# Performance work log

Hardware: AMD Instinct MI355X
Metric: run time of the kernel (lower is better)

The kernel has to match this reference:

```python
import jax, jax.numpy as jnp
import numpy as np

E, T, D_IN, D_H = 8, 4096, 2048, 1408

def setup_inputs() -> dict:
    key = jax.random.key(0)
    k_x, k_g, k_d, k_u = jax.random.split(key, 4)
    x = jax.random.normal(k_x, (E, T, D_IN), dtype=jnp.float32)
    gate_proj = jax.random.normal(k_g, (E, D_IN, D_H), dtype=jnp.float32) * 0.02
    down_proj = jax.random.normal(k_d, (E, D_IN, D_H), dtype=jnp.float32) * 0.02
    up_proj = jax.random.normal(k_u, (E, D_H, D_IN), dtype=jnp.float32) * 0.02
    return {"x": x, "gate_proj": gate_proj, "down_proj": down_proj,
            "up_proj": up_proj, "tokens_per_expert": T}

def reference(x, gate_proj, down_proj, up_proj, tokens_per_expert):
    # ep_size == 1 -> dispatch/combine are identity; x: [E, T, dim_in]
    # SwiGLU: h = silu(x @ gate) * (x @ down); out = h @ up
    h = jax.nn.silu(jnp.einsum('etd,edh->eth', x, gate_proj)) \
        * jnp.einsum('etd,edh->eth', x, down_proj)
    out = jnp.einsum('eth,ehd->etd', h, up_proj)
    return out
```

## Files before the change

kernel.cpp:

```cpp
#include <hip/hip_runtime.h>
#include <hip/hip_bf16.h>


typedef __bf16 bf16x8 __attribute__((ext_vector_type(8)));
typedef float  f32x4  __attribute__((ext_vector_type(4)));

__device__ __forceinline__ void gload16(const void* g, void* l) {
  __builtin_amdgcn_global_load_lds((const __attribute__((address_space(1))) void*)g,
                                   (__attribute__((address_space(3))) void*)l,
                                   16, 0, 0);
}

__device__ __forceinline__ unsigned short f2bf(float f) {
  union { float fv; unsigned u; } v; v.fv = f;
  unsigned r = (v.u + 0x7fffu + ((v.u >> 16) & 1u)) >> 16;
  return (unsigned short)r;
}

__global__ __launch_bounds__(256)
void cvt_f32_bf16(const float* __restrict__ in, unsigned short* __restrict__ out,
                  long n) {
  long i = ((long)blockIdx.x * 256 + threadIdx.x) * 4;
  const long stride = (long)gridDim.x * 1024;
  for (; i < n; i += stride) {
    const float4 v = *(const float4*)(in + i);
    ushort4 o;
    o.x = f2bf(v.x); o.y = f2bf(v.y); o.z = f2bf(v.z); o.w = f2bf(v.w);
    *(ushort4*)(out + i) = o;
  }
}

__global__ __launch_bounds__(256)
void trcvt(const float* __restrict__ in, unsigned short* __restrict__ out,
           int R, int C) {
  __shared__ unsigned short tile[32][33];
  const float* src = in + (size_t)blockIdx.z * R * C;
  unsigned short* dst = out + (size_t)blockIdx.z * R * C;
  const int c0 = blockIdx.x << 5, r0 = blockIdx.y << 5;
  const int tx = threadIdx.x, ty = threadIdx.y;
#pragma unroll
  for (int i = 0; i < 32; i += 8)
    tile[ty + i][tx] = f2bf(src[(size_t)(r0 + ty + i) * C + (c0 + tx)]);
  __syncthreads();
#pragma unroll
  for (int i = 0; i < 32; i += 8)
    dst[(size_t)(c0 + ty + i) * R + (r0 + tx)] = tile[tx][ty + i];
}

template <int KDIM, int NDIM, bool FUSED, bool F32OUT>
__global__ __launch_bounds__(512, 2)
void gemm_ring(const unsigned short* __restrict__ A,
               const unsigned short* __restrict__ B0,
               const unsigned short* __restrict__ B1,
               void* __restrict__ Cout) {
  constexpr int BN   = FUSED ? 128 : 256;
  constexpr int NB_N = NDIM / BN;
  constexpr int NS   = KDIM / 32;
  constexpr int SLOT = 16384;

  __shared__ __align__(16) unsigned short lds[4 * SLOT];

  const int t = threadIdx.x;
  const int w = t >> 6;
  const int lane = t & 63;
  const int e = blockIdx.y;

  const int cpx = gridDim.x >> 3;
  const int bid = (blockIdx.x & 7) * cpx + (blockIdx.x >> 3);
  const int m0 = (bid / NB_N) << 8;
  const int n0 = (bid % NB_N) * BN;

  const unsigned short* Ae  = A  + (size_t)e * 4096 * KDIM;
  const unsigned short* Be0 = B0 + (size_t)e * NDIM * KDIM;

  const int prow = lane >> 2;
  const int pcol = (((lane & 3) ^ ((lane >> 3) & 3)) << 3);

  const unsigned short* s0 = Ae + (size_t)(m0 + (w << 4) + prow) * KDIM + pcol;
  const unsigned short* s1 = Ae + (size_t)(m0 + ((w + 8) << 4) + prow) * KDIM + pcol;
  const unsigned short* s2;
  const unsigned short* s3;
  if constexpr (FUSED) {
    const unsigned short* Be1 = B1 + (size_t)e * NDIM * KDIM;
    s2 = Be0 + (size_t)(n0 + (w << 4) + prow) * KDIM + pcol;
    s3 = Be1 + (size_t)(n0 + (w << 4) + prow) * KDIM + pcol;
  } else {
    s2 = Be0 + (size_t)(n0 + (w << 4) + prow) * KDIM + pcol;
    s3 = Be0 + (size_t)(n0 + ((w + 8) << 4) + prow) * KDIM + pcol;
  }
  const int d0 = (w << 9);
  const int d1 = ((w + 8) << 9);
  const int d2 = 8192 + (w << 9);
  const int d3 = FUSED ? (12288 + (w << 9))
                       : (8192 + ((w + 8) << 9));

  auto stageA = [&](int slot) {
    unsigned short* b = &lds[slot * SLOT];
    gload16(s0, b + d0); s0 += 32;
    gload16(s1, b + d1); s1 += 32;
  };
  auto stageB = [&](int slot) {
    unsigned short* b = &lds[slot * SLOT];
    gload16(s2, b + d2); s2 += 32;
    gload16(s3, b + d3); s3 += 32;
  };

  const int wm = FUSED ? ((w >> 1) << 6) : ((w >> 2) << 7);
  const int wn = FUSED ? ((w & 1) << 6) : ((w & 3) << 6);
  const int apan = wm >> 4;
  const int bpan = wn >> 4;
  const int lm = lane & 15;
  const int kq = lane >> 4;
  const int fo = lm * 4 + (kq ^ ((lm >> 1) & 3));

  constexpr int NMI = FUSED ? 4 : 8;
  f32x4 acc0[NMI][4];
  f32x4 acc1[FUSED ? 4 : 1][4];
  const f32x4 z = {0.f, 0.f, 0.f, 0.f};
#pragma unroll
  for (int mi = 0; mi < NMI; ++mi)
#pragma unroll
    for (int nj = 0; nj < 4; ++nj) acc0[mi][nj] = z;
  if constexpr (FUSED) {
#pragma unroll
    for (int mi = 0; mi < 4; ++mi)
#pragma unroll
      for (int nj = 0; nj < 4; ++nj) acc1[mi][nj] = z;
  }

  bf16x8 af[4], bf0[4], bf1[4];

  stageA(0); stageB(0);
  stageA(1); stageB(1);
  stageA(2); stageB(2);
  asm volatile("s_waitcnt vmcnt(8)" ::: "memory");
  __builtin_amdgcn_s_barrier();

  for (int s = 0; s < NS; ++s) {
    const unsigned short* buf = &lds[(s & 3) * SLOT];
    const bf16x8* pA   = (const bf16x8*)buf;
    const bf16x8* pB   = (const bf16x8*)(buf + 8192);
    const bf16x8* pB1v = (const bf16x8*)(buf + 12288);
    const bool pf = (s + 3 < NS);
    const int ps = (s + 3) & 3;

#pragma unroll
    for (int mi = 0; mi < 4; ++mi) af[mi] = pA[(apan + mi) * 64 + fo];
#pragma unroll
    for (int nj = 0; nj < 4; ++nj) bf0[nj] = pB[(bpan + nj) * 64 + fo];
    if (pf) stageA(ps);
    __builtin_amdgcn_s_barrier();
    __builtin_amdgcn_s_setprio(1);
#pragma unroll
    for (int mi = 0; mi < 4; ++mi)
#pragma unroll
      for (int nj = 0; nj < 4; ++nj)
        acc0[mi][nj] = __builtin_amdgcn_mfma_f32_16x16x32_bf16(
            af[mi], bf0[nj], acc0[mi][nj], 0, 0, 0);
    __builtin_amdgcn_s_setprio(0);
    __builtin_amdgcn_s_barrier();

    if constexpr (FUSED) {
#pragma unroll
      for (int nj = 0; nj < 4; ++nj) bf1[nj] = pB1v[(bpan + nj) * 64 + fo];
    } else {
#pragma unroll
      for (int mi = 0; mi < 4; ++mi) af[mi] = pA[(apan + 4 + mi) * 64 + fo];
    }
    if (pf) stageB(ps);
    __builtin_amdgcn_s_barrier();
    __builtin_amdgcn_s_setprio(1);
    if constexpr (FUSED) {
#pragma unroll
      for (int mi = 0; mi < 4; ++mi)
#pragma unroll
        for (int nj = 0; nj < 4; ++nj)
          acc1[mi][nj] = __builtin_amdgcn_mfma_f32_16x16x32_bf16(
              af[mi], bf1[nj], acc1[mi][nj], 0, 0, 0);
    } else {
#pragma unroll
      for (int mi = 0; mi < 4; ++mi)
#pragma unroll
        for (int nj = 0; nj < 4; ++nj)
          acc0[4 + mi][nj] = __builtin_amdgcn_mfma_f32_16x16x32_bf16(
              af[mi], bf0[nj], acc0[4 + mi][nj], 0, 0, 0);
    }
    __builtin_amdgcn_s_setprio(0);
    if (s + 3 < NS)      asm volatile("s_waitcnt vmcnt(8)" ::: "memory");
    else if (s + 2 < NS) asm volatile("s_waitcnt vmcnt(4)" ::: "memory");
    else if (s + 1 < NS) asm volatile("s_waitcnt vmcnt(0)" ::: "memory");
    __builtin_amdgcn_s_barrier();
  }

  const size_t cbase = (size_t)e * 4096 * NDIM;
  if constexpr (F32OUT) {
    float* C = (float*)Cout + cbase;
#pragma unroll
    for (int mi = 0; mi < NMI; ++mi)
#pragma unroll
      for (int nj = 0; nj < 4; ++nj)
#pragma unroll
        for (int i = 0; i < 4; ++i) {
          const int row = m0 + wm + (mi << 4) + (kq << 2) + i;
          const int col = n0 + wn + (nj << 4) + lm;
          C[(size_t)row * NDIM + col] = acc0[mi][nj][i];
        }
  } else {
    unsigned short* C = (unsigned short*)Cout + cbase;
#pragma unroll
    for (int mi = 0; mi < 4; ++mi)
#pragma unroll
      for (int nj = 0; nj < 4; ++nj)
#pragma unroll
        for (int i = 0; i < 4; ++i) {
          const int row = m0 + wm + (mi << 4) + (kq << 2) + i;
          const int col = n0 + wn + (nj << 4) + lm;
          const float g = acc0[mi][nj][i];
          const float d = acc1[mi][nj][i];
          C[(size_t)row * NDIM + col] = f2bf(g / (1.0f + __expf(-g)) * d);
        }
  }
}

extern "C" void kernel_launch(void* const* d_in, const int* in_sizes, int n_in,
                              void* d_out, int out_size, void* d_ws, size_t ws_size,
                              hipStream_t stream) {
  const float* x    = (const float*)d_in[0];
  const float* gate = (const float*)d_in[1];
  const float* down = (const float*)d_in[2];
  const float* up   = (const float*)d_in[3];

  unsigned short* xb = (unsigned short*)d_out;

  char* ws = (char*)d_ws;
  unsigned short* h    = (unsigned short*)ws;
  unsigned short* bufG = (unsigned short*)(ws + 92274688ull);
  unsigned short* bufD = (unsigned short*)(ws + 138412032ull);

  const long nx = 8L * 4096 * 2048;
  cvt_f32_bf16<<<8192, 256, 0, stream>>>(x, xb, nx);

  dim3 tb(32, 8, 1);
  trcvt<<<dim3(44, 64, 8), tb, 0, stream>>>(gate, bufG, 2048, 1408);
  trcvt<<<dim3(44, 64, 8), tb, 0, stream>>>(down, bufD, 2048, 1408);

  gemm_ring<2048, 1408, true, false><<<dim3(176, 8), 512, 0, stream>>>(xb, bufG, bufD, h);

  trcvt<<<dim3(64, 44, 8), tb, 0, stream>>>(up, bufG, 1408, 2048);

  gemm_ring<1408, 2048, false, true><<<dim3(128, 8), 512, 0, stream>>>(h, bufG, nullptr, (float*)d_out);
}
```

Before: 1.184 ms.

## Double-buffer LDS fragments in GEMM main loop and enlarge transpose tiles

The GEMM main loop now issues the next stage's A/B fragment reads from LDS into alternate register sets while the second MFMA batch of the current stage runs. This cuts the barriers per k-step from three to one and merges the A and B prefetches into a single stage call. The transpose-convert kernel moves to 64x64 tiles with 512 threads to lower launch and per-block overhead. In exchange the GEMM uses more registers and has a subtler ordering of waitcnt and barrier against the LDS slot being overwritten.

```diff
diff --git a/kernel.cpp b/kernel.cpp
--- a/kernel.cpp
+++ b/kernel.cpp
@@ -30,20 +30,20 @@
   }
 }
 
-__global__ __launch_bounds__(256)
+__global__ __launch_bounds__(512)
 void trcvt(const float* __restrict__ in, unsigned short* __restrict__ out,
            int R, int C) {
-  __shared__ unsigned short tile[32][33];
+  __shared__ unsigned short tile[64][65];
   const float* src = in + (size_t)blockIdx.z * R * C;
   unsigned short* dst = out + (size_t)blockIdx.z * R * C;
-  const int c0 = blockIdx.x << 5, r0 = blockIdx.y << 5;
+  const int c0 = blockIdx.x << 6, r0 = blockIdx.y << 6;
   const int tx = threadIdx.x, ty = threadIdx.y;
 #pragma unroll
-  for (int i = 0; i < 32; i += 8)
+  for (int i = 0; i < 64; i += 8)
     tile[ty + i][tx] = f2bf(src[(size_t)(r0 + ty + i) * C + (c0 + tx)]);
   __syncthreads();
 #pragma unroll
-  for (int i = 0; i < 32; i += 8)
+  for (int i = 0; i < 64; i += 8)
     dst[(size_t)(c0 + ty + i) * R + (r0 + tx)] = tile[tx][ty + i];
 }
 
@@ -91,16 +91,12 @@
   const int d0 = (w << 9);
   const int d1 = ((w + 8) << 9);
   const int d2 = 8192 + (w << 9);
-  const int d3 = FUSED ? (12288 + (w << 9))
-                       : (8192 + ((w + 8) << 9));
-
-  auto stageA = [&](int slot) {
+  const int d3 = FUSED ? (12288 + (w << 9)) : (8192 + ((w + 8) << 9));
+
+  auto stage = [&](int slot) {
     unsigned short* b = &lds[slot * SLOT];
     gload16(s0, b + d0); s0 += 32;
     gload16(s1, b + d1); s1 += 32;
-  };
-  auto stageB = [&](int slot) {
-    unsigned short* b = &lds[slot * SLOT];
     gload16(s2, b + d2); s2 += 32;
     gload16(s3, b + d3); s3 += 32;
   };
@@ -128,69 +124,77 @@
       for (int nj = 0; nj < 4; ++nj) acc1[mi][nj] = z;
   }
 
-  bf16x8 af[4], bf0[4], bf1[4];
-
-  stageA(0); stageB(0);
-  stageA(1); stageB(1);
-  stageA(2); stageB(2);
+  bf16x8 afX[4], afY[4];
+  bf16x8 bfX[4], bfY[4];
+  bf16x8 g1[4];
+
+  stage(0); stage(1); stage(2);
   asm volatile("s_waitcnt vmcnt(8)" ::: "memory");
   __builtin_amdgcn_s_barrier();
-
-  for (int s = 0; s < NS; ++s) {
-    const unsigned short* buf = &lds[(s & 3) * SLOT];
-    const bf16x8* pA   = (const bf16x8*)buf;
-    const bf16x8* pB   = (const bf16x8*)(buf + 8192);
-    const bf16x8* pB1v = (const bf16x8*)(buf + 12288);
-    const bool pf = (s + 3 < NS);
-    const int ps = (s + 3) & 3;
-
-#pragma unroll
-    for (int mi = 0; mi < 4; ++mi) af[mi] = pA[(apan + mi) * 64 + fo];
-#pragma unroll
-    for (int nj = 0; nj < 4; ++nj) bf0[nj] = pB[(bpan + nj) * 64 + fo];
-    if (pf) stageA(ps);
-    __builtin_amdgcn_s_barrier();
-    __builtin_amdgcn_s_setprio(1);
-#pragma unroll
-    for (int mi = 0; mi < 4; ++mi)
-#pragma unroll
-      for (int nj = 0; nj < 4; ++nj)
-        acc0[mi][nj] = __builtin_amdgcn_mfma_f32_16x16x32_bf16(
-            af[mi], bf0[nj], acc0[mi][nj], 0, 0, 0);
-    __builtin_amdgcn_s_setprio(0);
-    __builtin_amdgcn_s_barrier();
-
-    if constexpr (FUSED) {
-#pragma unroll
-      for (int nj = 0; nj < 4; ++nj) bf1[nj] = pB1v[(bpan + nj) * 64 + fo];
-    } else {
-#pragma unroll
-      for (int mi = 0; mi < 4; ++mi) af[mi] = pA[(apan + 4 + mi) * 64 + fo];
-    }
-    if (pf) stageB(ps);
-    __builtin_amdgcn_s_barrier();
-    __builtin_amdgcn_s_setprio(1);
-    if constexpr (FUSED) {
-#pragma unroll
-      for (int mi = 0; mi < 4; ++mi)
-#pragma unroll
-        for (int nj = 0; nj < 4; ++nj)
-          acc1[mi][nj] = __builtin_amdgcn_mfma_f32_16x16x32_bf16(
-              af[mi], bf1[nj], acc1[mi][nj], 0, 0, 0);
-    } else {
-#pragma unroll
-      for (int mi = 0; mi < 4; ++mi)
-#pragma unroll
-        for (int nj = 0; nj < 4; ++nj)
-          acc0[4 + mi][nj] = __builtin_amdgcn_mfma_f32_16x16x32_bf16(
-              af[mi], bf0[nj], acc0[4 + mi][nj], 0, 0, 0);
-    }
-    __builtin_amdgcn_s_setprio(0);
-    if (s + 3 < NS)      asm volatile("s_waitcnt vmcnt(8)" ::: "memory");
-    else if (s + 2 < NS) asm volatile("s_waitcnt vmcnt(4)" ::: "memory");
-    else if (s + 1 < NS) asm volatile("s_waitcnt vmcnt(0)" ::: "memory");
-    __builtin_amdgcn_s_barrier();
-  }
+  {
+    const bf16x8* pA = (const bf16x8*)&lds[0];
+    const bf16x8* pB = (const bf16x8*)&lds[8192];
+#pragma unroll
+    for (int mi = 0; mi < 4; ++mi) afX[mi] = pA[(apan + mi) * 64 + fo];
+#pragma unroll
+    for (int nj = 0; nj < 4; ++nj) bfX[nj] = pB[(bpan + nj) * 64 + fo];
+  }
+
+#define STEP(S, AFC, AFN, BFC, BFN)                                            \
+  {                                                                            \
+    const int s_ = (S);                                                        \
+    const unsigned short* buf = &lds[(s_ & 3) * SLOT];                         \
+                      \
+    if constexpr (FUSED) {                                                     \
+      const bf16x8* pB1 = (const bf16x8*)(buf + 12288);                        \
+      _Pragma("unroll") for (int nj = 0; nj < 4; ++nj)                         \
+        g1[nj] = pB1[(bpan + nj) * 64 + fo];                                   \
+    } else {                                                                   \
+      const bf16x8* pA = (const bf16x8*)buf;                                   \
+      _Pragma("unroll") for (int mi = 0; mi < 4; ++mi)                         \
+        g1[mi] = pA[(apan + 4 + mi) * 64 + fo];                                \
+    }                                                                          \
+    __builtin_amdgcn_s_setprio(1);                                             \
+    _Pragma("unroll") for (int mi = 0; mi < 4; ++mi)                           \
+      _Pragma("unroll") for (int nj = 0; nj < 4; ++nj)                         \
+        acc0[mi][nj] = __builtin_amdgcn_mfma_f32_16x16x32_bf16(                \
+            AFC[mi], BFC[nj], acc0[mi][nj], 0, 0, 0);                          \
+    __builtin_amdgcn_s_setprio(0);                                             \
+        \
+    if (s_ < NS - 2)      asm volatile("s_waitcnt vmcnt(4)" ::: "memory");     \
+    else if (s_ < NS - 1) asm volatile("s_waitcnt vmcnt(0)" ::: "memory");     \
+    if (s_ < NS - 1) __builtin_amdgcn_s_barrier();                             \
+    if (s_ + 3 < NS) stage((s_ + 3) & 3);                                      \
+                          \
+    if (s_ < NS - 1) {                                                         \
+      const unsigned short* nbuf = &lds[((s_ + 1) & 3) * SLOT];                \
+      const bf16x8* pAn = (const bf16x8*)nbuf;                                 \
+      const bf16x8* pBn = (const bf16x8*)(nbuf + 8192);                        \
+      _Pragma("unroll") for (int mi = 0; mi < 4; ++mi)                         \
+        AFN[mi] = pAn[(apan + mi) * 64 + fo];                                  \
+      _Pragma("unroll") for (int nj = 0; nj < 4; ++nj)                         \
+        BFN[nj] = pBn[(bpan + nj) * 64 + fo];                                  \
+    }                                                                          \
+    __builtin_amdgcn_s_setprio(1);                                             \
+    if constexpr (FUSED) {                                                     \
+      _Pragma("unroll") for (int mi = 0; mi < 4; ++mi)                         \
+        _Pragma("unroll") for (int nj = 0; nj < 4; ++nj)                       \
+          acc1[mi][nj] = __builtin_amdgcn_mfma_f32_16x16x32_bf16(              \
+              AFC[mi], g1[nj], acc1[mi][nj], 0, 0, 0);                         \
+    } else {                                                                   \
+      _Pragma("unroll") for (int mi = 0; mi < 4; ++mi)                         \
+        _Pragma("unroll") for (int nj = 0; nj < 4; ++nj)                       \
+          acc0[4 + mi][nj] = __builtin_amdgcn_mfma_f32_16x16x32_bf16(          \
+              g1[mi], BFC[nj], acc0[4 + mi][nj], 0, 0, 0);                     \
+    }                                                                          \
+    __builtin_amdgcn_s_setprio(0);                                             \
+  }
+
+  for (int s = 0; s < NS; s += 2) {
+    STEP(s,     afX, afY, bfX, bfY)
+    STEP(s + 1, afY, afX, bfY, bfX)
+  }
+#undef STEP
 
   const size_t cbase = (size_t)e * 4096 * NDIM;
   if constexpr (F32OUT) {
@@ -240,13 +244,13 @@
   const long nx = 8L * 4096 * 2048;
   cvt_f32_bf16<<<8192, 256, 0, stream>>>(x, xb, nx);
 
-  dim3 tb(32, 8, 1);
-  trcvt<<<dim3(44, 64, 8), tb, 0, stream>>>(gate, bufG, 2048, 1408);
-  trcvt<<<dim3(44, 64, 8), tb, 0, stream>>>(down, bufD, 2048, 1408);
+  dim3 tb(64, 8, 1);
+  trcvt<<<dim3(22, 32, 8), tb, 0, stream>>>(gate, bufG, 2048, 1408);
+  trcvt<<<dim3(22, 32, 8), tb, 0, stream>>>(down, bufD, 2048, 1408);
 
   gemm_ring<2048, 1408, true, false><<<dim3(176, 8), 512, 0, stream>>>(xb, bufG, bufD, h);
 
-  trcvt<<<dim3(64, 44, 8), tb, 0, stream>>>(up, bufG, 1408, 2048);
+  trcvt<<<dim3(32, 22, 8), tb, 0, stream>>>(up, bufG, 1408, 2048);
 
   gemm_ring<1408, 2048, false, true><<<dim3(128, 8), 512, 0, stream>>>(h, bufG, nullptr, (float*)d_out);
 }
```

New measurement: 1.167 ms. No clear change (-1.4%).
